# Performance work log

Measured on AMD Instinct MI355X. Metric: run time of the kernel, lower is better.

Reference implementation:

```python
import jax, jax.numpy as jnp
import numpy as np

E = 2048
H = 16
DH = E // H  # 128
B, T = 2, 2048
EPS = 1e-8


def rmsnorm(x, g):
    rms = jnp.sqrt(jnp.mean(x * x, axis=-1, keepdims=True) + EPS)
    return g * (x / rms)


def setup_inputs() -> dict:
    key = jax.random.key(0)
    ks = jax.random.split(key, 16)
    s_in = 1.0 / np.sqrt(E)
    s_ff = 1.0 / np.sqrt(4 * E)
    return {
        "x": jax.random.normal(ks[0], (B, T, E), dtype=jnp.float32),
        # stacked per-head QKV projections, stored (in, out) so y = x @ W + b
        "wq": jax.random.normal(ks[1], (H, E, DH), dtype=jnp.float32) * s_in,
        "bq": jax.random.normal(ks[2], (H, DH), dtype=jnp.float32) * s_in,
        "wk": jax.random.normal(ks[3], (H, E, DH), dtype=jnp.float32) * s_in,
        "bk": jax.random.normal(ks[4], (H, DH), dtype=jnp.float32) * s_in,
        "wv": jax.random.normal(ks[5], (H, E, DH), dtype=jnp.float32) * s_in,
        "bv": jax.random.normal(ks[6], (H, DH), dtype=jnp.float32) * s_in,
        "wo": jax.random.normal(ks[7], (E, E), dtype=jnp.float32) * s_in,
        "bo": jax.random.normal(ks[8], (E,), dtype=jnp.float32) * s_in,
        "w1": jax.random.normal(ks[9], (E, 4 * E), dtype=jnp.float32) * s_in,
        "b1": jax.random.normal(ks[10], (4 * E,), dtype=jnp.float32) * s_in,
        "w2": jax.random.normal(ks[11], (4 * E, E), dtype=jnp.float32) * s_ff,
        "b2": jax.random.normal(ks[12], (E,), dtype=jnp.float32) * s_ff,
        "g1": jnp.ones((E,), dtype=jnp.float32),
        "g2": jnp.ones((E,), dtype=jnp.float32),
    }


def reference(x, wq, bq, wk, bk, wv, bv, wo, bo, w1, b1, w2, b2, g1, g2):
    b, t, e = x.shape
    # --- attention sublayer ---
    h = rmsnorm(x, g1)
    q = jnp.einsum("bte,hed->bhtd", h, wq) + bq[None, :, None, :]
    k = jnp.einsum("bte,hed->bhtd", h, wk) + bk[None, :, None, :]
    v = jnp.einsum("bte,hed->bhtd", h, wv) + bv[None, :, None, :]
    scores = jnp.einsum("bhtd,bhsd->bhts", q, k) / jnp.sqrt(jnp.float32(DH))
    causal = jnp.tril(jnp.ones((t, t), dtype=bool))
    scores = jnp.where(causal[None, None], scores, -jnp.inf)
    w = jax.nn.softmax(scores, axis=-1)
    o = jnp.einsum("bhts,bhsd->bhtd", w, v)
    o = o.transpose(0, 2, 1, 3).reshape(b, t, e)  # concat heads on last dim
    x = x + o @ wo + bo
    # --- FFN sublayer (exact GELU, dropout is identity at inference) ---
    h = rmsnorm(x, g2)
    x = x + jax.nn.gelu(h @ w1 + b1, approximate=False) @ w2 + b2
    return x
```

## Files before the change

kernel.cpp:

```cpp
#include <hip/hip_runtime.h>
#include <hip/hip_bf16.h>

typedef unsigned short u16;
typedef unsigned int   u32;
typedef __attribute__((ext_vector_type(8))) short short8;
typedef __attribute__((ext_vector_type(4))) float f32x4;
typedef __attribute__((ext_vector_type(4))) unsigned short u16x4;

#define E_    2048
#define H_    16
#define DH_   128
#define B_    2
#define T_    2048
#define NTOK  4096
#define QKVN  6144

#define VMCNT(n) asm volatile("s_waitcnt vmcnt(" #n ")" ::: "memory")

__device__ __forceinline__ u16 f2bf(float f) {
  union { float f; u32 u; } v; v.f = f;
  u32 r = (v.u + 0x7FFFu + ((v.u >> 16) & 1u)) >> 16;
  return (u16)r;
}

__global__ __launch_bounds__(256) void tr64(
    const float* __restrict__ in, u16* __restrict__ out,
    int R, int C, size_t inZ, size_t outZ)
{
  __shared__ float t[64][65];
  const float* ib = in + (size_t)blockIdx.z * inZ;
  u16* ob = out + (size_t)blockIdx.z * outZ;
  const int r0 = blockIdx.y * 64, c0 = blockIdx.x * 64;
  const int tid = threadIdx.x;
  const int rr = tid >> 4;
  const int cc = (tid & 15) * 4;
  #pragma unroll
  for (int p = 0; p < 4; ++p) {
    const float4 v = *(const float4*)(ib + (size_t)(r0 + p * 16 + rr) * C + c0 + cc);
    t[cc + 0][p * 16 + rr] = v.x;
    t[cc + 1][p * 16 + rr] = v.y;
    t[cc + 2][p * 16 + rr] = v.z;
    t[cc + 3][p * 16 + rr] = v.w;
  }
  __syncthreads();
  const int wr = tid >> 3;
  const int wc = (tid & 7) * 8;
  #pragma unroll
  for (int p = 0; p < 2; ++p) {
    short8 s;
    #pragma unroll
    for (int j = 0; j < 8; ++j) s[j] = (short)f2bf(t[p * 32 + wr][wc + j]);
    *(short8*)(ob + (size_t)(c0 + p * 32 + wr) * R + r0 + wc) = s;
  }
}

__global__ __launch_bounds__(256) void bias_cat(
    const float* __restrict__ bq, const float* __restrict__ bk,
    const float* __restrict__ bv, float* __restrict__ bias)
{
  int idx = blockIdx.x * 256 + threadIdx.x;
  const float* bb = (idx < 2048) ? bq : (idx < 4096) ? bk : bv;
  bias[idx] = bb[idx & 2047];
}

__global__ __launch_bounds__(256) void rmsnorm_k(
    const float* __restrict__ x, const float* __restrict__ g, u16* __restrict__ o)
{
  const int row = blockIdx.x;
  const float4* xr = (const float4*)(x + (size_t)row * E_);
  const float4* gr = (const float4*)g;
  const int tid = threadIdx.x;
  float4 a0 = xr[tid], a1 = xr[tid + 256];
  float s = a0.x*a0.x + a0.y*a0.y + a0.z*a0.z + a0.w*a0.w
          + a1.x*a1.x + a1.y*a1.y + a1.z*a1.z + a1.w*a1.w;
  #pragma unroll
  for (int m = 1; m < 64; m <<= 1) s += __shfl_xor(s, m);
  __shared__ float wsum[4];
  if ((tid & 63) == 0) wsum[tid >> 6] = s;
  __syncthreads();
  float tot = wsum[0] + wsum[1] + wsum[2] + wsum[3];
  float rinv = rsqrtf(tot * (1.0f / E_) + 1e-8f);
  float4 g0 = gr[tid], g1 = gr[tid + 256];
  u16x4 o0, o1;
  o0[0] = f2bf(a0.x * g0.x * rinv); o0[1] = f2bf(a0.y * g0.y * rinv);
  o0[2] = f2bf(a0.z * g0.z * rinv); o0[3] = f2bf(a0.w * g0.w * rinv);
  o1[0] = f2bf(a1.x * g1.x * rinv); o1[1] = f2bf(a1.y * g1.y * rinv);
  o1[2] = f2bf(a1.z * g1.z * rinv); o1[3] = f2bf(a1.w * g1.w * rinv);
  u16x4* orow = (u16x4*)(o + (size_t)row * E_);
  orow[tid] = o0;
  orow[tid + 256] = o1;
}

__device__ __forceinline__ void gload_lds16(const void* g, u16* lds_base) {
  __builtin_amdgcn_global_load_lds(
      (const __attribute__((address_space(1))) u32*)g,
      (__attribute__((address_space(3))) u32*)lds_base, 16, 0, 0);
}

template<int BM, int BN, int MODE, int EPI>
__global__ __launch_bounds__(512, 2)
void gemm3(const u16* __restrict__ A, const u16* __restrict__ Bt,
           const float* __restrict__ bias, const float* __restrict__ resid,
           void* __restrict__ out, int M, int N, int K)
{
  constexpr int WROWS = BM / 2;
  constexpr int WCOLS = BN / 4;
  constexpr int MR    = WROWS / 16;
  constexpr int BUF   = (BM + BN) * 32;
  __shared__ __align__(16) u16 sh[3 * BUF];

  const int tid  = threadIdx.x;
  const int lane = tid & 63;
  const int l15  = lane & 15, lg = lane >> 4;
  const int w    = tid >> 6;
  const int wm   = w >> 2;
  const int wn   = w & 3;
  const int xs   = (l15 >> 1) & 3;

  const int nbx = N / BN;
  const int nwg = nbx * (M / BM);
  const int q8  = nwg >> 3;
  const int xcd = blockIdx.x & 7, j = blockIdx.x >> 3;
  int m0, n0;
  if constexpr (MODE == 1) {
    const int ncx = nbx >> 3;
    n0 = (xcd * ncx + j % ncx) * BN;
    m0 = (j / ncx) * BM;
  } else {
    const int sid = xcd * q8 + j;
    m0 = (sid / nbx) * BM;
    n0 = (sid % nbx) * BN;
  }

  const int r0 = tid >> 2;
  const int c0 = (((tid & 3) ^ ((tid >> 3) & 3)) * 8);
  const u16* gA  = A  + (size_t)(m0 + r0) * K + c0;
  const u16* gB  = Bt + (size_t)(n0 + r0) * K + c0;
  const u16* gA2 = gA + (size_t)128 * K;
  const u16* gB2 = gB + (size_t)128 * K;
  const int wub = (tid & ~63) * 8;

  f32x4 acc[MR][4] = {};
  const int NT = K >> 5;

  #pragma unroll
  for (int t = 0; t < 2; ++t) {
    u16* wb = sh + t * BUF;
    const int kS = t * 32;
    if constexpr (BM == 256) {
      gload_lds16(gA  + kS, wb + wub);
      gload_lds16(gA2 + kS, wb + 512 * 8 + wub);
      gload_lds16(gB  + kS, wb + 1024 * 8 + wub);
      gload_lds16(gB2 + kS, wb + 1536 * 8 + wub);
    } else {
      gload_lds16(gA  + kS, wb + wub);
      gload_lds16(gB  + kS, wb + 512 * 8 + wub);
      gload_lds16(gB2 + kS, wb + 1024 * 8 + wub);
    }
  }
  if constexpr (BM == 256) VMCNT(4); else VMCNT(3);
  __builtin_amdgcn_s_barrier();

  int i = 0;

#define KTILE(CUR, STG)                                                          \
  do {                                                                           \
    const u16* rb = sh + (CUR) * BUF;                                            \
    u16* wb = sh + (STG) * BUF;                                                  \
    const bool st = (i + 2 < NT);                                                \
    const int kS = (i + 2) << 5;                                                 \
    const int rem = NT - 1 - i;                                                  \
    short8 af[4], bf[4];                                                         \
    if constexpr (BM == 256) {                                                   \
      _Pragma("unroll")                                                          \
      for (int n = 0; n < 4; ++n)                                                \
        bf[n] = *(const short8*)(rb + BM * 32 + (wn * WCOLS + n * 16 + l15) * 32 + ((lg ^ xs) * 8)); \
      _Pragma("unroll")                                                          \
      for (int m = 0; m < 4; ++m)                                                \
        af[m] = *(const short8*)(rb + (wm * WROWS + m * 16 + l15) * 32 + ((lg ^ xs) * 8)); \
      if (st) {                                                                  \
        gload_lds16(gA + kS, wb + wub);                                          \
        gload_lds16(gB + kS, wb + 1024 * 8 + wub);                               \
      }                                                                          \
      __builtin_amdgcn_s_barrier();                                              \
      __builtin_amdgcn_s_setprio(1);                                             \
      _Pragma("unroll")                                                          \
      for (int m = 0; m < 4; ++m)                                                \
        _Pragma("unroll")                                                        \
        for (int n = 0; n < 4; ++n)                                              \
          acc[m][n] = __builtin_amdgcn_mfma_f32_16x16x32_bf16(af[m], bf[n], acc[m][n], 0, 0, 0); \
      __builtin_amdgcn_s_setprio(0);                                             \
      __builtin_amdgcn_s_barrier();                                              \
      _Pragma("unroll")                                                          \
      for (int m = 0; m < 4; ++m)                                                \
        af[m] = *(const short8*)(rb + (wm * WROWS + (4 + m) * 16 + l15) * 32 + ((lg ^ xs) * 8)); \
      if (st) {                                                                  \
        gload_lds16(gA2 + kS, wb + 512 * 8 + wub);                               \
        gload_lds16(gB2 + kS, wb + 1536 * 8 + wub);                              \
      }                                                                          \
      __builtin_amdgcn_s_barrier();                                              \
      __builtin_amdgcn_s_setprio(1);                                             \
      _Pragma("unroll")                                                          \
      for (int m = 0; m < 4; ++m)                                                \
        _Pragma("unroll")                                                        \
        for (int n = 0; n < 4; ++n)                                              \
          acc[4 + m][n] = __builtin_amdgcn_mfma_f32_16x16x32_bf16(af[m], bf[n], acc[4 + m][n], 0, 0, 0); \
      __builtin_amdgcn_s_setprio(0);                                             \
      if (rem >= 2) { VMCNT(4); } else { VMCNT(0); }                             \
      __builtin_amdgcn_s_barrier();                                              \
    } else {                                                                     \
      _Pragma("unroll")                                                          \
      for (int n = 0; n < 4; ++n)                                                \
        bf[n] = *(const short8*)(rb + BM * 32 + (wn * WCOLS + n * 16 + l15) * 32 + ((lg ^ xs) * 8)); \
      _Pragma("unroll")                                                          \
      for (int m = 0; m < 4; ++m)                                                \
        af[m] = *(const short8*)(rb + (wm * WROWS + m * 16 + l15) * 32 + ((lg ^ xs) * 8)); \
      if (st) {                                                                  \
        gload_lds16(gA  + kS, wb + wub);                                         \
        gload_lds16(gB  + kS, wb + 512 * 8 + wub);                               \
        gload_lds16(gB2 + kS, wb + 1024 * 8 + wub);                              \
      }                                                                          \
      __builtin_amdgcn_s_barrier();                                              \
      __builtin_amdgcn_s_setprio(1);                                             \
      _Pragma("unroll")                                                          \
      for (int m = 0; m < 4; ++m)                                                \
        _Pragma("unroll")                                                        \
        for (int n = 0; n < 4; ++n)                                              \
          acc[m][n] = __builtin_amdgcn_mfma_f32_16x16x32_bf16(af[m], bf[n], acc[m][n], 0, 0, 0); \
      __builtin_amdgcn_s_setprio(0);                                             \
      if (rem >= 2) { VMCNT(3); } else { VMCNT(0); }                             \
      __builtin_amdgcn_s_barrier();                                              \
    }                                                                            \
    ++i;                                                                         \
  } while (0)

  const int trips = NT / 3;
  #pragma unroll 1
  for (int t = 0; t < trips; ++t) {
    KTILE(0, 2);
    KTILE(1, 0);
    KTILE(2, 1);
  }
  if (i < NT) KTILE(0, 2);
  if (i < NT) KTILE(1, 0);
#undef KTILE

  float bv[4];
  #pragma unroll
  for (int n = 0; n < 4; ++n) bv[n] = bias[n0 + wn * WCOLS + n * 16 + l15];

  if constexpr (EPI == 1) {
    #pragma unroll
    for (int n = 0; n < 4; ++n) {
      const int col = n0 + wn * WCOLS + n * 16 + l15;
      #pragma unroll
      for (int m = 0; m < MR; ++m)
        #pragma unroll
        for (int r = 0; r < 4; ++r) {
          const int row = m0 + wm * WROWS + m * 16 + lg * 4 + r;
          const size_t off = (size_t)row * N + col;
          ((float*)out)[off] = acc[m][n][r] + bv[n] + resid[off];
        }
    }
  } else {
    u16* ep = sh + w * 1024;
    #pragma unroll
    for (int m = 0; m < MR; ++m) {
      #pragma unroll
      for (int n = 0; n < 4; ++n)
        #pragma unroll
        for (int r = 0; r < 4; ++r) {
          float v = acc[m][n][r] + bv[n];
          if (EPI == 2) v = 0.5f * v * (1.0f + erff(v * 0.70710678118654752f));
          ep[(lg * 4 + r) * 64 + n * 16 + l15] = f2bf(v);
        }
      asm volatile("s_waitcnt lgkmcnt(0)" ::: "memory");
      const int row0 = m0 + wm * WROWS + m * 16;
      #pragma unroll
      for (int it = 0; it < 2; ++it) {
        const int ch = it * 64 + lane;
        const int rr = ch >> 3, c8 = ch & 7;
        short8 s = *(const short8*)(ep + rr * 64 + c8 * 8);
        *(short8*)((u16*)out + (size_t)(row0 + rr) * N + n0 + wn * WCOLS + c8 * 8) = s;
      }
      asm volatile("s_waitcnt lgkmcnt(0)" ::: "memory");
    }
  }
}

__global__ __launch_bounds__(256) void vtrans_k(
    const u16* __restrict__ qkv, u16* __restrict__ vt)
{
  __shared__ u16 tile[DH_][66];
  const int tid = threadIdx.x;
  const int bid = blockIdx.x;
  const int tt = bid & 31;
  const int bh = bid >> 5;
  const int b  = bh >> 4, h = bh & 15;
  const int t0 = tt * 64;
  const u16* src = qkv + (size_t)b * T_ * QKVN + 2 * E_ + h * DH_;
  #pragma unroll
  for (int it = 0; it < 8; ++it) {
    int c = it * 256 + tid;
    int t = c >> 5, dc = c & 31;
    u16x4 v = *(const u16x4*)(src + (size_t)(t0 + t) * QKVN + dc * 4);
    #pragma unroll
    for (int j = 0; j < 4; ++j) tile[dc * 4 + j][t] = v[j];
  }
  __syncthreads();
  u16* dst = vt + (size_t)bh * DH_ * T_ + t0;
  #pragma unroll
  for (int it = 0; it < 8; ++it) {
    int c = it * 256 + tid;
    int d = c >> 4, tc = c & 15;
    u16x4 v;
    #pragma unroll
    for (int j = 0; j < 4; ++j) v[j] = tile[d][tc * 4 + j];
    *(u16x4*)(dst + (size_t)d * T_ + tc * 4) = v;
  }
}

__global__ __launch_bounds__(256) void attn_k(
    const u16* __restrict__ qkv, const u16* __restrict__ vt, u16* __restrict__ o)
{
  const int tid  = threadIdx.x;
  const int lane = tid & 63;
  const int w    = tid >> 6;
  const int l15  = lane & 15, lg = lane >> 4;
  const int bid  = blockIdx.x;
  const int pair = bid & 31;
  const int qt   = 15 - (bid >> 5);
  const int h    = pair & 15;
  const int b    = pair >> 4;
  const int Q0 = qt * 128;
  const int qw = Q0 + w * 32;

  __shared__ __align__(16) u16 Ks[2][64 * 128];
  __shared__ __align__(16) u16 Vs[2][128 * 64];
  __shared__ __align__(16) u16 Ps[4][32 * 64];

  const u16* qb  = qkv + (size_t)b * T_ * QKVN + h * DH_;
  const u16* kb  = qb + E_;
  const u16* vtb = vt + (size_t)(b * H_ + h) * DH_ * T_;

  short8 qf[2][4];
  #pragma unroll
  for (int qi = 0; qi < 2; ++qi)
    #pragma unroll
    for (int kk = 0; kk < 4; ++kk)
      qf[qi][kk] = *(const short8*)(qb + (size_t)(qw + qi * 16 + l15) * QKVN + kk * 32 + lg * 8);

  f32x4 oacc[2][8] = {};
  float m_[2][4], l_[2][4];
  #pragma unroll
  for (int qi = 0; qi < 2; ++qi)
    #pragma unroll
    for (int r = 0; r < 4; ++r) { m_[qi][r] = -1e30f; l_[qi][r] = 0.f; }

  const int xr = l15 & 7;
  const float scl = 0.08838834764831845f;
  const int nt = Q0 / 64 + 2;
  const int qmaxw = qw + 31;
  const int wub = (tid & ~63);

  const u16* kp[4]; const u16* vp[4];
  #pragma unroll
  for (int i = 0; i < 4; ++i) {
    int f = i * 256 + tid;
    int r = f >> 4, p = f & 15, c = p ^ (r & 7);
    kp[i] = kb + (size_t)r * QKVN + c * 8;
  }
  #pragma unroll
  for (int i = 0; i < 4; ++i) {
    int f = i * 256 + tid;
    int d = f >> 3, p = f & 7, c = p ^ (d & 7);
    vp[i] = vtb + (size_t)d * T_ + c * 8;
  }

  auto STAGEKV = [&](int s0, int bufi) {
    const size_t ko = (size_t)s0 * QKVN;
    #pragma unroll
    for (int i = 0; i < 4; ++i)
      gload_lds16(kp[i] + ko, &Ks[bufi][(i * 256 + wub) * 8]);
    #pragma unroll
    for (int i = 0; i < 4; ++i)
      gload_lds16(vp[i] + s0, &Vs[bufi][(i * 256 + wub) * 8]);
  };

  STAGEKV(0, 0);
  VMCNT(0);
  __builtin_amdgcn_s_barrier();

  #pragma unroll 1
  for (int st = 0; st < nt; ++st) {
    const int s0 = st * 64;
    const int cur = st & 1;
    if (st + 1 < nt) STAGEKV(s0 + 64, cur ^ 1);

    if (s0 <= qmaxw) {
      const u16* Kc = Ks[cur];
      const u16* Vc = Vs[cur];
      f32x4 sc[2][4] = {};
      __builtin_amdgcn_s_setprio(1);
      #pragma unroll
      for (int sj = 0; sj < 4; ++sj) {
        const int row = sj * 16 + l15;
        #pragma unroll
        for (int kk = 0; kk < 4; ++kk) {
          short8 kfr = *(const short8*)(Kc + row * 128 + (((kk * 4 + lg) ^ xr) * 8));
          sc[0][sj] = __builtin_amdgcn_mfma_f32_16x16x32_bf16(qf[0][kk], kfr, sc[0][sj], 0, 0, 0);
          sc[1][sj] = __builtin_amdgcn_mfma_f32_16x16x32_bf16(qf[1][kk], kfr, sc[1][sj], 0, 0, 0);
        }
      }
      __builtin_amdgcn_s_setprio(0);
      const bool needmask = (s0 + 63 > qw);
      #pragma unroll
      for (int qi = 0; qi < 2; ++qi)
        #pragma unroll
        for (int sj = 0; sj < 4; ++sj)
          #pragma unroll
          for (int r = 0; r < 4; ++r) {
            float v = sc[qi][sj][r] * scl;
            if (needmask) {
              int s = s0 + sj * 16 + l15;
              int q = qw + qi * 16 + lg * 4 + r;
              if (s > q) v = -1e30f;
            }
            sc[qi][sj][r] = v;
          }
      #pragma unroll
      for (int qi = 0; qi < 2; ++qi) {
        float tmax[4], alpha[4], rsum[4];
        #pragma unroll
        for (int r = 0; r < 4; ++r)
          tmax[r] = fmaxf(fmaxf(sc[qi][0][r], sc[qi][1][r]), fmaxf(sc[qi][2][r], sc[qi][3][r]));
        #pragma unroll
        for (int r = 0; r < 4; ++r)
          #pragma unroll
          for (int m = 1; m < 16; m <<= 1) tmax[r] = fmaxf(tmax[r], __shfl_xor(tmax[r], m));
        #pragma unroll
        for (int r = 0; r < 4; ++r) {
          float mn = fmaxf(m_[qi][r], tmax[r]);
          alpha[r] = __expf(m_[qi][r] - mn);
          m_[qi][r] = mn;
          rsum[r] = 0.f;
        }
        #pragma unroll
        for (int sj = 0; sj < 4; ++sj)
          #pragma unroll
          for (int r = 0; r < 4; ++r) {
            float p = __expf(sc[qi][sj][r] - m_[qi][r]);
            rsum[r] += p;
            const int row = qi * 16 + lg * 4 + r;
            const int ch  = (sj * 2 + (l15 >> 3)) ^ (row & 7);
            Ps[w][row * 64 + ch * 8 + (l15 & 7)] = f2bf(p);
          }
        #pragma unroll
        for (int r = 0; r < 4; ++r) {
          #pragma unroll
          for (int m = 1; m < 16; m <<= 1) rsum[r] += __shfl_xor(rsum[r], m);
          l_[qi][r] = l_[qi][r] * alpha[r] + rsum[r];
        }
        #pragma unroll
        for (int dj = 0; dj < 8; ++dj)
          #pragma unroll
          for (int r = 0; r < 4; ++r) oacc[qi][dj][r] *= alpha[r];
      }
      __builtin_amdgcn_s_setprio(1);
      #pragma unroll
      for (int ks = 0; ks < 2; ++ks) {
        short8 pf0 = *(const short8*)(&Ps[w][l15 * 64 + (((ks * 4 + lg) ^ xr) * 8)]);
        short8 pf1 = *(const short8*)(&Ps[w][(16 + l15) * 64 + (((ks * 4 + lg) ^ xr) * 8)]);
        #pragma unroll
        for (int dj = 0; dj < 8; ++dj) {
          const int row = dj * 16 + l15;
          short8 vfr = *(const short8*)(Vc + row * 64 + (((ks * 4 + lg) ^ xr) * 8));
          oacc[0][dj] = __builtin_amdgcn_mfma_f32_16x16x32_bf16(pf0, vfr, oacc[0][dj], 0, 0, 0);
          oacc[1][dj] = __builtin_amdgcn_mfma_f32_16x16x32_bf16(pf1, vfr, oacc[1][dj], 0, 0, 0);
        }
      }
      __builtin_amdgcn_s_setprio(0);
    }
    VMCNT(0);
    __builtin_amdgcn_s_barrier();
  }

  float inv[2][4];
  #pragma unroll
  for (int qi = 0; qi < 2; ++qi)
    #pragma unroll
    for (int r = 0; r < 4; ++r) inv[qi][r] = 1.0f / l_[qi][r];
  u16* ob = o + (size_t)(b * T_ + qw) * E_ + h * DH_;
  #pragma unroll
  for (int qi = 0; qi < 2; ++qi)
    #pragma unroll
    for (int dj = 0; dj < 8; ++dj)
      #pragma unroll
      for (int r = 0; r < 4; ++r)
        ob[(size_t)(qi * 16 + lg * 4 + r) * E_ + dj * 16 + l15] = f2bf(oacc[qi][dj][r] * inv[qi][r]);
}

extern "C" void kernel_launch(void* const* d_in, const int* in_sizes, int n_in,
                              void* d_out, int out_size, void* d_ws, size_t ws_size,
                              hipStream_t stream)
{
  const float* x  = (const float*)d_in[0];
  const float* wq = (const float*)d_in[1];
  const float* bq = (const float*)d_in[2];
  const float* wk = (const float*)d_in[3];
  const float* bk = (const float*)d_in[4];
  const float* wv = (const float*)d_in[5];
  const float* bv = (const float*)d_in[6];
  const float* wo = (const float*)d_in[7];
  const float* bo = (const float*)d_in[8];
  const float* w1 = (const float*)d_in[9];
  const float* b1 = (const float*)d_in[10];
  const float* w2 = (const float*)d_in[11];
  const float* b2 = (const float*)d_in[12];
  const float* g1 = (const float*)d_in[13];
  const float* g2 = (const float*)d_in[14];
  float* xout = (float*)d_out;

  if (ws_size < 201351168u) return;

  char* ws = (char*)d_ws;
  u16*   wqkv_t = (u16*)(ws + 0);
  u16*   h1     = (u16*)(ws + 25165824);
  u16*   qkv    = (u16*)(ws + 41943040);
  u16*   vt     = (u16*)(ws + 92274688);
  u16*   o_     = (u16*)(ws + 109051904);
  u16*   wo_t   = (u16*)(ws + 125829120);
  u16*   w1_t   = (u16*)(ws + 134217728);
  u16*   w2_t   = (u16*)(ws + 167772160);
  float* bqkv   = (float*)(ws + 201326592);
  u16*   u_     = (u16*)(ws + 0);
  u16*   h2     = vt;
  float* x2     = xout;

  tr64<<<dim3(2, 32, 16), 256, 0, stream>>>(wq, wqkv_t,                          E_, DH_, (size_t)E_ * DH_, (size_t)DH_ * E_);
  tr64<<<dim3(2, 32, 16), 256, 0, stream>>>(wk, wqkv_t + (size_t)E_ * E_,        E_, DH_, (size_t)E_ * DH_, (size_t)DH_ * E_);
  tr64<<<dim3(2, 32, 16), 256, 0, stream>>>(wv, wqkv_t + (size_t)2 * E_ * E_,    E_, DH_, (size_t)E_ * DH_, (size_t)DH_ * E_);
  tr64<<<dim3(32, 32, 1),  256, 0, stream>>>(wo, wo_t, E_, E_, 0, 0);
  tr64<<<dim3(128, 32, 1), 256, 0, stream>>>(w1, w1_t, E_, 4 * E_, 0, 0);
  tr64<<<dim3(32, 128, 1), 256, 0, stream>>>(w2, w2_t, 4 * E_, E_, 0, 0);
  bias_cat<<<24, 256, 0, stream>>>(bq, bk, bv, bqkv);

  rmsnorm_k<<<NTOK, 256, 0, stream>>>(x, g1, h1);
  gemm3<128, 256, 1, 0><<<(NTOK / 128) * (QKVN / 256), 512, 0, stream>>>(h1, wqkv_t, bqkv, nullptr, qkv, NTOK, QKVN, E_);
  vtrans_k<<<B_ * H_ * (T_ / 64), 256, 0, stream>>>(qkv, vt);
  attn_k<<<B_ * H_ * (T_ / 16 / 8), 256, 0, stream>>>(qkv, vt, o_);
  gemm3<128, 256, 0, 1><<<(NTOK / 128) * (E_ / 256), 512, 0, stream>>>(o_, wo_t, bo, x, x2, NTOK, E_, E_);
  rmsnorm_k<<<NTOK, 256, 0, stream>>>(x2, g2, h2);
  gemm3<256, 256, 1, 2><<<(NTOK / 256) * (4 * E_ / 256), 512, 0, stream>>>(h2, w1_t, b1, nullptr, u_, NTOK, 4 * E_, E_);
  gemm3<128, 256, 0, 1><<<(NTOK / 128) * (E_ / 256), 512, 0, stream>>>(u_, w2_t, b2, x2, xout, NTOK, E_, 4 * E_);
}
```

Baseline: 700.6 us.

## Add 256x256 double-buffered GEMM with 64-wide K steps for QKV and FFN1

Adds a gemm8 kernel that uses 256x256 tiles, a 64-element K step split into two 32-wide halves, and two 64 KB LDS buffers instead of the triple-buffered 32-wide scheme. The QKV projection moves from 128x256 tiles to 256x256, and FFN1 moves to the new kernel. gemm3 is reduced to its BM=128 path. The aim is more arithmetic per tile load and fewer barrier phases per unit of K, at the cost of 128 KB of LDS per block, which likely limits occupancy to one block per CU despite launch_bounds(512,2), plus added lgkmcnt waits.

New measurement: 705.9 us. No clear change (+0.8%).

```diff
diff --git a/kernel.cpp b/kernel.cpp
--- a/kernel.cpp
+++ b/kernel.cpp
@@ -16,6 +16,7 @@
 #define QKVN  6144
 
 #define VMCNT(n) asm volatile("s_waitcnt vmcnt(" #n ")" ::: "memory")
+#define LGKM0()  asm volatile("s_waitcnt lgkmcnt(0)" ::: "memory")
 
 __device__ __forceinline__ u16 f2bf(float f) {
   union { float f; u32 u; } v; v.f = f;
@@ -97,6 +98,187 @@
       (__attribute__((address_space(3))) u32*)lds_base, 16, 0, 0);
 }
 
+template<int MODE, int EPI>
+__global__ __launch_bounds__(512, 2)
+void gemm8(const u16* __restrict__ A, const u16* __restrict__ Bt,
+           const float* __restrict__ bias, const float* __restrict__ resid,
+           void* __restrict__ out, int M, int N, int K)
+{
+  __shared__ __align__(16) u16 sh[2 * 32768];
+
+  const int tid  = threadIdx.x;
+  const int lane = tid & 63;
+  const int l15  = lane & 15, lg = lane >> 4;
+  const int w    = tid >> 6;
+  const int wm   = w >> 2;
+  const int wn   = w & 3;
+  const int xs   = (l15 >> 1) & 3;
+
+  const int nbx = N / 256;
+  const int xcd = blockIdx.x & 7, j = blockIdx.x >> 3;
+  int m0, n0;
+  if constexpr (MODE == 1) {
+    const int ncx = nbx >> 3;
+    n0 = (xcd * ncx + j % ncx) * 256;
+    m0 = (j / ncx) * 256;
+  } else {
+    const int nwg = nbx * (M / 256);
+    const int sid = xcd * (nwg >> 3) + j;
+    m0 = (sid / nbx) * 256;
+    n0 = (sid % nbx) * 256;
+  }
+
+  const int r0 = tid >> 2;
+  const int c0 = (((tid & 3) ^ ((tid >> 3) & 3)) * 8);
+  const u16* gA  = A  + (size_t)(m0 + r0) * K + c0;
+  const u16* gB  = Bt + (size_t)(n0 + r0) * K + c0;
+  const u16* gA2 = gA + (size_t)128 * K;
+  const u16* gB2 = gB + (size_t)128 * K;
+  const int wub = (tid & ~63) * 8;
+
+  f32x4 acc[8][4] = {};
+  const int NT = K >> 6;
+  int g = 0;
+
+  gload_lds16(gA,       sh + wub);             gload_lds16(gA2,      sh + 4096  + wub);
+  gload_lds16(gB,       sh + 16384 + wub);     gload_lds16(gB2,      sh + 20480 + wub);
+  gload_lds16(gA  + 32, sh + 8192  + wub);     gload_lds16(gA2 + 32, sh + 12288 + wub);
+  gload_lds16(gB  + 32, sh + 24576 + wub);     gload_lds16(gB2 + 32, sh + 28672 + wub);
+  VMCNT(4);
+  __builtin_amdgcn_s_barrier();
+
+#define TILE8(CUR)                                                                \
+  do {                                                                            \
+    const u16* rbA0 = sh + (CUR) * 32768;                                         \
+    const u16* rbA1 = rbA0 + 8192;                                                \
+    const u16* rbB0 = rbA0 + 16384;                                               \
+    const u16* rbB1 = rbA0 + 24576;                                               \
+    u16* wbuf = sh + (1 - (CUR)) * 32768;                                         \
+    const bool st = (g + 1 < NT);                                                 \
+    const size_t kS = (size_t)(g + 1) << 6;                                       \
+    short8 af[4], bf[4];                                                          \
+                                                     \
+    _Pragma("unroll")                                                             \
+    for (int n = 0; n < 4; ++n)                                                   \
+      bf[n] = *(const short8*)(rbB0 + (wn * 64 + n * 16 + l15) * 32 + ((lg ^ xs) * 8)); \
+    _Pragma("unroll")                                                             \
+    for (int m = 0; m < 4; ++m)                                                   \
+      af[m] = *(const short8*)(rbA0 + (wm * 128 + m * 16 + l15) * 32 + ((lg ^ xs) * 8)); \
+    if (st) { gload_lds16(gA + kS, wbuf + wub); gload_lds16(gA2 + kS, wbuf + 4096 + wub); } \
+    __builtin_amdgcn_s_barrier();                                                 \
+    LGKM0();                                                                      \
+    __builtin_amdgcn_s_setprio(1);                                                \
+    _Pragma("unroll")                                                             \
+    for (int m = 0; m < 4; ++m)                                                   \
+      _Pragma("unroll")                                                           \
+      for (int n = 0; n < 4; ++n)                                                 \
+        acc[m][n] = __builtin_amdgcn_mfma_f32_16x16x32_bf16(af[m], bf[n], acc[m][n], 0, 0, 0); \
+    __builtin_amdgcn_s_setprio(0);                                                \
+    __builtin_amdgcn_s_barrier();                                                 \
+                                                     \
+    _Pragma("unroll")                                                             \
+    for (int m = 0; m < 4; ++m)                                                   \
+      af[m] = *(const short8*)(rbA0 + (wm * 128 + 64 + m * 16 + l15) * 32 + ((lg ^ xs) * 8)); \
+    if (st) { gload_lds16(gB + kS, wbuf + 16384 + wub); gload_lds16(gB2 + kS, wbuf + 20480 + wub); } \
+    __builtin_amdgcn_s_barrier();                                                 \
+    LGKM0();                                                                      \
+    __builtin_amdgcn_s_setprio(1);                                                \
+    _Pragma("unroll")                                                             \
+    for (int m = 0; m < 4; ++m)                                                   \
+      _Pragma("unroll")                                                           \
+      for (int n = 0; n < 4; ++n)                                                 \
+        acc[4 + m][n] = __builtin_amdgcn_mfma_f32_16x16x32_bf16(af[m], bf[n], acc[4 + m][n], 0, 0, 0); \
+    __builtin_amdgcn_s_setprio(0);                                                \
+    if (st) { VMCNT(4); } else { VMCNT(0); }                                      \
+    __builtin_amdgcn_s_barrier();                                                 \
+                                                     \
+    _Pragma("unroll")                                                             \
+    for (int n = 0; n < 4; ++n)                                                   \
+      bf[n] = *(const short8*)(rbB1 + (wn * 64 + n * 16 + l15) * 32 + ((lg ^ xs) * 8)); \
+    _Pragma("unroll")                                                             \
+    for (int m = 0; m < 4; ++m)                                                   \
+      af[m] = *(const short8*)(rbA1 + (wm * 128 + m * 16 + l15) * 32 + ((lg ^ xs) * 8)); \
+    if (st) { gload_lds16(gA + kS + 32, wbuf + 8192 + wub); gload_lds16(gA2 + kS + 32, wbuf + 12288 + wub); } \
+    __builtin_amdgcn_s_barrier();                                                 \
+    LGKM0();                                                                      \
+    __builtin_amdgcn_s_setprio(1);                                                \
+    _Pragma("unroll")                                                             \
+    for (int m = 0; m < 4; ++m)                                                   \
+      _Pragma("unroll")                                                           \
+      for (int n = 0; n < 4; ++n)                                                 \
+        acc[m][n] = __builtin_amdgcn_mfma_f32_16x16x32_bf16(af[m], bf[n], acc[m][n], 0, 0, 0); \
+    __builtin_amdgcn_s_setprio(0);                                                \
+    __builtin_amdgcn_s_barrier();                                                 \
+                                                     \
+    _Pragma("unroll")                                                             \
+    for (int m = 0; m < 4; ++m)                                                   \
+      af[m] = *(const short8*)(rbA1 + (wm * 128 + 64 + m * 16 + l15) * 32 + ((lg ^ xs) * 8)); \
+    if (st) { gload_lds16(gB + kS + 32, wbuf + 24576 + wub); gload_lds16(gB2 + kS + 32, wbuf + 28672 + wub); } \
+    __builtin_amdgcn_s_barrier();                                                 \
+    LGKM0();                                                                      \
+    __builtin_amdgcn_s_setprio(1);                                                \
+    _Pragma("unroll")                                                             \
+    for (int m = 0; m < 4; ++m)                                                   \
+      _Pragma("unroll")                                                           \
+      for (int n = 0; n < 4; ++n)                                                 \
+        acc[4 + m][n] = __builtin_amdgcn_mfma_f32_16x16x32_bf16(af[m], bf[n], acc[4 + m][n], 0, 0, 0); \
+    __builtin_amdgcn_s_setprio(0);                                                \
+    if (st) { VMCNT(4); } else { VMCNT(0); }                                      \
+    __builtin_amdgcn_s_barrier();                                                 \
+    ++g;                                                                          \
+  } while (0)
+
+  const int pairs = NT >> 1;
+  #pragma unroll 1
+  for (int t = 0; t < pairs; ++t) {
+    TILE8(0);
+    TILE8(1);
+  }
+#undef TILE8
+
+  float bv[4];
+  #pragma unroll
+  for (int n = 0; n < 4; ++n) bv[n] = bias[n0 + wn * 64 + n * 16 + l15];
+
+  if constexpr (EPI == 1) {
+    #pragma unroll
+    for (int n = 0; n < 4; ++n) {
+      const int col = n0 + wn * 64 + n * 16 + l15;
+      #pragma unroll
+      for (int m = 0; m < 8; ++m)
+        #pragma unroll
+        for (int r = 0; r < 4; ++r) {
+          const int row = m0 + wm * 128 + m * 16 + lg * 4 + r;
+          const size_t off = (size_t)row * N + col;
+          ((float*)out)[off] = acc[m][n][r] + bv[n] + resid[off];
+        }
+    }
+  } else {
+    u16* ep = sh + w * 1024;
+    #pragma unroll
+    for (int m = 0; m < 8; ++m) {
+      #pragma unroll
+      for (int n = 0; n < 4; ++n)
+        #pragma unroll
+        for (int r = 0; r < 4; ++r) {
+          float v = acc[m][n][r] + bv[n];
+          if (EPI == 2) v = 0.5f * v * (1.0f + erff(v * 0.70710678118654752f));
+          ep[(lg * 4 + r) * 64 + n * 16 + l15] = f2bf(v);
+        }
+      LGKM0();
+      const int row0 = m0 + wm * 128 + m * 16;
+      #pragma unroll
+      for (int it = 0; it < 2; ++it) {
+        const int ch = it * 64 + lane;
+        const int rr = ch >> 3, c8 = ch & 7;
+        short8 s = *(const short8*)(ep + rr * 64 + c8 * 8);
+        *(short8*)((u16*)out + (size_t)(row0 + rr) * N + n0 + wn * 64 + c8 * 8) = s;
+      }
+      LGKM0();
+    }
+  }
+}
+
 template<int BM, int BN, int MODE, int EPI>
 __global__ __launch_bounds__(512, 2)
 void gemm3(const u16* __restrict__ A, const u16* __restrict__ Bt,
@@ -136,7 +318,6 @@
   const int c0 = (((tid & 3) ^ ((tid >> 3) & 3)) * 8);
   const u16* gA  = A  + (size_t)(m0 + r0) * K + c0;
   const u16* gB  = Bt + (size_t)(n0 + r0) * K + c0;
-  const u16* gA2 = gA + (size_t)128 * K;
   const u16* gB2 = gB + (size_t)128 * K;
   const int wub = (tid & ~63) * 8;
 
@@ -147,18 +328,11 @@
   for (int t = 0; t < 2; ++t) {
     u16* wb = sh + t * BUF;
     const int kS = t * 32;
-    if constexpr (BM == 256) {
-      gload_lds16(gA  + kS, wb + wub);
-      gload_lds16(gA2 + kS, wb + 512 * 8 + wub);
-      gload_lds16(gB  + kS, wb + 1024 * 8 + wub);
-      gload_lds16(gB2 + kS, wb + 1536 * 8 + wub);
-    } else {
-      gload_lds16(gA  + kS, wb + wub);
-      gload_lds16(gB  + kS, wb + 512 * 8 + wub);
-      gload_lds16(gB2 + kS, wb + 1024 * 8 + wub);
-    }
-  }
-  if constexpr (BM == 256) VMCNT(4); else VMCNT(3);
+    gload_lds16(gA  + kS, wb + wub);
+    gload_lds16(gB  + kS, wb + 512 * 8 + wub);
+    gload_lds16(gB2 + kS, wb + 1024 * 8 + wub);
+  }
+  VMCNT(3);
   __builtin_amdgcn_s_barrier();
 
   int i = 0;
@@ -171,66 +345,27 @@
     const int kS = (i + 2) << 5;                                                 \
     const int rem = NT - 1 - i;                                                  \
     short8 af[4], bf[4];                                                         \
-    if constexpr (BM == 256) {                                                   \
+    _Pragma("unroll")                                                            \
+    for (int n = 0; n < 4; ++n)                                                  \
+      bf[n] = *(const short8*)(rb + BM * 32 + (wn * WCOLS + n * 16 + l15) * 32 + ((lg ^ xs) * 8)); \
+    _Pragma("unroll")                                                            \
+    for (int m = 0; m < 4; ++m)                                                  \
+      af[m] = *(const short8*)(rb + (wm * WROWS + m * 16 + l15) * 32 + ((lg ^ xs) * 8)); \
+    if (st) {                                                                    \
+      gload_lds16(gA  + kS, wb + wub);                                           \
+      gload_lds16(gB  + kS, wb + 512 * 8 + wub);                                 \
+      gload_lds16(gB2 + kS, wb + 1024 * 8 + wub);                                \
+    }                                                                            \
+    __builtin_amdgcn_s_barrier();                                                \
+    __builtin_amdgcn_s_setprio(1);                                               \
+    _Pragma("unroll")                                                            \
+    for (int m = 0; m < 4; ++m)                                                  \
       _Pragma("unroll")                                                          \
       for (int n = 0; n < 4; ++n)                                                \
-        bf[n] = *(const short8*)(rb + BM * 32 + (wn * WCOLS + n * 16 + l15) * 32 + ((lg ^ xs) * 8)); \
-      _Pragma("unroll")                                                          \
-      for (int m = 0; m < 4; ++m)                                                \
-        af[m] = *(const short8*)(rb + (wm * WROWS + m * 16 + l15) * 32 + ((lg ^ xs) * 8)); \
-      if (st) {                                                                  \
-        gload_lds16(gA + kS, wb + wub);                                          \
-        gload_lds16(gB + kS, wb + 1024 * 8 + wub);                               \
-      }                                                                          \
-      __builtin_amdgcn_s_barrier();                                              \
-      __builtin_amdgcn_s_setprio(1);                                             \
-      _Pragma("unroll")                                                          \
-      for (int m = 0; m < 4; ++m)                                                \
-        _Pragma("unroll")                                                        \
-        for (int n = 0; n < 4; ++n)                                              \
-          acc[m][n] = __builtin_amdgcn_mfma_f32_16x16x32_bf16(af[m], bf[n], acc[m][n], 0, 0, 0); \
-      __builtin_amdgcn_s_setprio(0);                                             \
-      __builtin_amdgcn_s_barrier();                                              \
-      _Pragma("unroll")                                                          \
-      for (int m = 0; m < 4; ++m)                                                \
-        af[m] = *(const short8*)(rb + (wm * WROWS + (4 + m) * 16 + l15) * 32 + ((lg ^ xs) * 8)); \
-      if (st) {                                                                  \
-        gload_lds16(gA2 + kS, wb + 512 * 8 + wub);                               \
-        gload_lds16(gB2 + kS, wb + 1536 * 8 + wub);                              \
-      }                                                                          \
-      __builtin_amdgcn_s_barrier();                                              \
-      __builtin_amdgcn_s_setprio(1);                                             \
-      _Pragma("unroll")                                                          \
-      for (int m = 0; m < 4; ++m)                                                \
-        _Pragma("unroll")                                                        \
-        for (int n = 0; n < 4; ++n)                                              \
-          acc[4 + m][n] = __builtin_amdgcn_mfma_f32_16x16x32_bf16(af[m], bf[n], acc[4 + m][n], 0, 0, 0); \
-      __builtin_amdgcn_s_setprio(0);                                             \
-      if (rem >= 2) { VMCNT(4); } else { VMCNT(0); }                             \
-      __builtin_amdgcn_s_barrier();                                              \
-    } else {                                                                     \
-      _Pragma("unroll")                                                          \
-      for (int n = 0; n < 4; ++n)                                                \
-        bf[n] = *(const short8*)(rb + BM * 32 + (wn * WCOLS + n * 16 + l15) * 32 + ((lg ^ xs) * 8)); \
-      _Pragma("unroll")                                                          \
-      for (int m = 0; m < 4; ++m)                                                \
-        af[m] = *(const short8*)(rb + (wm * WROWS + m * 16 + l15) * 32 + ((lg ^ xs) * 8)); \
-      if (st) {                                                                  \
-        gload_lds16(gA  + kS, wb + wub);                                         \
-        gload_lds16(gB  + kS, wb + 512 * 8 + wub);                               \
-        gload_lds16(gB2 + kS, wb + 1024 * 8 + wub);                              \
-      }                                                                          \
-      __builtin_amdgcn_s_barrier();                                              \
-      __builtin_amdgcn_s_setprio(1);                                             \
-      _Pragma("unroll")                                                          \
-      for (int m = 0; m < 4; ++m)                                                \
-        _Pragma("unroll")                                                        \
-        for (int n = 0; n < 4; ++n)                                              \
-          acc[m][n] = __builtin_amdgcn_mfma_f32_16x16x32_bf16(af[m], bf[n], acc[m][n], 0, 0, 0); \
-      __builtin_amdgcn_s_setprio(0);                                             \
-      if (rem >= 2) { VMCNT(3); } else { VMCNT(0); }                             \
-      __builtin_amdgcn_s_barrier();                                              \
-    }                                                                            \
+        acc[m][n] = __builtin_amdgcn_mfma_f32_16x16x32_bf16(af[m], bf[n], acc[m][n], 0, 0, 0); \
+    __builtin_amdgcn_s_setprio(0);                                               \
+    if (rem >= 2) { VMCNT(3); } else { VMCNT(0); }                               \
+    __builtin_amdgcn_s_barrier();                                                \
     ++i;                                                                         \
   } while (0)
 
@@ -274,7 +409,7 @@
           if (EPI == 2) v = 0.5f * v * (1.0f + erff(v * 0.70710678118654752f));
           ep[(lg * 4 + r) * 64 + n * 16 + l15] = f2bf(v);
         }
-      asm volatile("s_waitcnt lgkmcnt(0)" ::: "memory");
+      LGKM0();
       const int row0 = m0 + wm * WROWS + m * 16;
       #pragma unroll
       for (int it = 0; it < 2; ++it) {
@@ -283,7 +418,7 @@
         short8 s = *(const short8*)(ep + rr * 64 + c8 * 8);
         *(short8*)((u16*)out + (size_t)(row0 + rr) * N + n0 + wn * WCOLS + c8 * 8) = s;
       }
-      asm volatile("s_waitcnt lgkmcnt(0)" ::: "memory");
+      LGKM0();
     }
   }
 }
@@ -546,11 +681,11 @@
   bias_cat<<<24, 256, 0, stream>>>(bq, bk, bv, bqkv);
 
   rmsnorm_k<<<NTOK, 256, 0, stream>>>(x, g1, h1);
-  gemm3<128, 256, 1, 0><<<(NTOK / 128) * (QKVN / 256), 512, 0, stream>>>(h1, wqkv_t, bqkv, nullptr, qkv, NTOK, QKVN, E_);
+  gemm8<1, 0><<<(NTOK / 256) * (QKVN / 256), 512, 0, stream>>>(h1, wqkv_t, bqkv, nullptr, qkv, NTOK, QKVN, E_);
   vtrans_k<<<B_ * H_ * (T_ / 64), 256, 0, stream>>>(qkv, vt);
   attn_k<<<B_ * H_ * (T_ / 16 / 8), 256, 0, stream>>>(qkv, vt, o_);
   gemm3<128, 256, 0, 1><<<(NTOK / 128) * (E_ / 256), 512, 0, stream>>>(o_, wo_t, bo, x, x2, NTOK, E_, E_);
   rmsnorm_k<<<NTOK, 256, 0, stream>>>(x2, g2, h2);
-  gemm3<256, 256, 1, 2><<<(NTOK / 256) * (4 * E_ / 256), 512, 0, stream>>>(h2, w1_t, b1, nullptr, u_, NTOK, 4 * E_, E_);
+  gemm8<1, 2><<<(NTOK / 256) * (4 * E_ / 256), 512, 0, stream>>>(h2, w1_t, b1, nullptr, u_, NTOK, 4 * E_, E_);
   gemm3<128, 256, 0, 1><<<(NTOK / 128) * (E_ / 256), 512, 0, stream>>>(u_, w2_t, b2, x2, xout, NTOK, E_, 4 * E_);
 }
```
